# Performance work log

Hardware: AMD Instinct MI355X
Metric: run time of the kernel (lower is better)

The kernel has to match this reference:

```python
import jax, jax.numpy as jnp
import numpy as np

ACT_DIM = 768
DICT_SIZE = 32768
S0 = 4096          # top-level latent size (dict_size // prod(lower sizes))
S1 = 8             # lower_level_latent_sizes[0]
K = 64             # per-token top-k (applied globally as k * batch)


def setup_inputs() -> dict:
    key = jax.random.key(0)
    ks = jax.random.split(key, 7)
    scale_e = 1.0 / np.sqrt(ACT_DIM)
    scale_d = 1.0 / np.sqrt(DICT_SIZE)
    return {
        "x": jax.random.normal(ks[0], (4096, ACT_DIM), dtype=jnp.float32),
        "W0": jax.random.normal(ks[1], (S0, ACT_DIM), dtype=jnp.float32) * scale_e,
        "b0": jnp.zeros((S0,), dtype=jnp.float32),
        "W1": jax.random.normal(ks[2], (DICT_SIZE, ACT_DIM), dtype=jnp.float32) * scale_e,
        "b1": jnp.zeros((DICT_SIZE,), dtype=jnp.float32),
        "Wd": jax.random.normal(ks[3], (ACT_DIM, DICT_SIZE), dtype=jnp.float32) * scale_d,
        "b_dec": jnp.zeros((ACT_DIM,), dtype=jnp.float32),
    }


def reference(x, W0, b0, W1, b1, Wd, b_dec):
    B = x.shape[0]
    x_centered = x - b_dec                                   # [B, D]
    # hierarchical relu encoders
    l0 = jax.nn.relu(x_centered @ W0.T + b0)                 # [B, S0]
    l1 = jax.nn.relu(x_centered @ W1.T + b1)                 # [B, S0*S1]
    # multiplicative gating: lower-level gate broadcast over finest level
    final_dense = (l1.reshape(B, S0, S1) * l0[:, :, None]).reshape(B, S0 * S1)
    # global batch top-k over flattened [B * dict_size]
    flat = final_dense.reshape(-1)
    k_for_batch = min(K * B, flat.shape[0])
    vals, idx = jax.lax.top_k(flat, k_for_batch)
    sparse_flat = jnp.zeros_like(flat).at[idx].set(vals)
    encoded = sparse_flat.reshape(B, S0 * S1)
    # decode
    x_hat = encoded @ Wd.T + b_dec                           # [B, D]
    return x_hat
```

## Files before the change

kernel.cpp:

```cpp
#include <hip/hip_runtime.h>
#include <stdint.h>

#define DDIM 768
#define BROWS 4096
#define S0N 4096
#define DICT 32768
#define KTOT 262144u
#define PREF 2.0f
#define DELTA 4e-3f
#define CAND_CAP 8388608u
#define BAND_CAP 4096

static constexpr size_t OFF_XH   = 0;
static constexpr size_t OFF_XL   = 6291456;
static constexpr size_t OFF_W0H  = 12582912;
static constexpr size_t OFF_W0L  = 18874368;
static constexpr size_t OFF_W1H  = 25165824;
static constexpr size_t OFF_W1L  = 75497472;
static constexpr size_t OFF_WDT  = 0;
static constexpr size_t OFF_L0   = 125829120;
static constexpr size_t OFF_CTRL = 192937984;
static constexpr size_t OFF_ROWC = 193069056;
static constexpr size_t OFF_ROWD = 193085440;
static constexpr size_t OFF_CAND = 201474048;
static constexpr size_t WS_NEED  = 268582912;


typedef __attribute__((ext_vector_type(8))) short bf16x8;
typedef __attribute__((ext_vector_type(4))) float f32x4;

__device__ __forceinline__ unsigned umin_(unsigned a, unsigned b) { return a < b ? a : b; }
__device__ __forceinline__ float relu_(float v) { return v > 0.f ? v : 0.f; }

__device__ __forceinline__ unsigned short f2bf(float f) {
    union { float f; unsigned u; } v; v.f = f;
    unsigned r = v.u + 0x7FFFu + ((v.u >> 16) & 1u);
    return (unsigned short)(r >> 16);
}
__device__ __forceinline__ float bf2f(unsigned short h) {
    union { float f; unsigned u; } v; v.u = ((unsigned)h) << 16;
    return v.f;
}
__device__ __forceinline__ void split1(float a, short& h, short& l) {
    unsigned short hb = f2bf(a);
    float rem = a - bf2f(hb);
    h = (short)hb;
    l = (short)f2bf(rem);
}

__device__ __forceinline__ void gl16(const void* g, void* l) {
    __builtin_amdgcn_global_load_lds(
        (const __attribute__((address_space(1))) void*)g,
        (__attribute__((address_space(3))) void*)l,
        16, 0, 0);
}

__global__ void k_split_x(const float* __restrict__ x, const float* __restrict__ b_dec,
                          short* __restrict__ XH, short* __restrict__ XL) {
    int i = blockIdx.x * 256 + threadIdx.x;
    float4 xv = ((const float4*)x)[i];
    int d = (i % (DDIM / 4)) * 4;
    float4 bv = *(const float4*)(b_dec + d);
    float a[4] = {xv.x - bv.x, xv.y - bv.y, xv.z - bv.z, xv.w - bv.w};
    short4 h, lo;
    split1(a[0], h.x, lo.x); split1(a[1], h.y, lo.y);
    split1(a[2], h.z, lo.z); split1(a[3], h.w, lo.w);
    ((short4*)XH)[i] = h;
    ((short4*)XL)[i] = lo;
}

__global__ void k_split_w(const float* __restrict__ W, short* __restrict__ H,
                          short* __restrict__ L) {
    int i = blockIdx.x * 256 + threadIdx.x;
    float4 wv = ((const float4*)W)[i];
    short4 h, lo;
    split1(wv.x, h.x, lo.x); split1(wv.y, h.y, lo.y);
    split1(wv.z, h.z, lo.z); split1(wv.w, h.w, lo.w);
    ((short4*)H)[i] = h;
    ((short4*)L)[i] = lo;
}

__global__ void k_transpose(const float* __restrict__ Wd, float* __restrict__ WdT) {
    __shared__ float tile[32][33];
    int j0 = blockIdx.x * 32, d0 = blockIdx.y * 32;
    int tx = threadIdx.x & 31, ty = threadIdx.x >> 5;
#pragma unroll
    for (int i = 0; i < 4; ++i)
        tile[ty + i * 8][tx] = Wd[(size_t)(d0 + ty + i * 8) * DICT + j0 + tx];
    __syncthreads();
#pragma unroll
    for (int i = 0; i < 4; ++i)
        WdT[(size_t)(j0 + ty + i * 8) * DDIM + d0 + tx] = tile[tx][ty + i * 8];
}

template<int EPI>
__launch_bounds__(256, 2) __global__
void k_mm(const short* __restrict__ XH, const short* __restrict__ XL,
          const short* __restrict__ WH, const short* __restrict__ WL,
          const float* __restrict__ bias, float* __restrict__ l0buf,
          uint2* __restrict__ cand, unsigned* __restrict__ ctrl) {
    __shared__ short sAH[4096], sAL[4096], sBH[4096], sBL[4096];
    __shared__ unsigned pscan[256];
    __shared__ unsigned basev;

    const int t = threadIdx.x;
    const int w = t >> 6, l = t & 63;
    const int wm = w >> 1, wn = w & 1;
    const int bm = blockIdx.y << 7, bn = blockIdx.x << 7;

    const size_t aoff = (size_t)(bm + (t >> 2)) * DDIM + ((t & 3) << 3);
    const size_t boff = (size_t)(bn + (t >> 2)) * DDIM + ((t & 3) << 3);
    const size_t rstep = (size_t)64 * DDIM;
    short* dA0h = &sAH[t * 8]; short* dA1h = &sAH[t * 8 + 2048];
    short* dA0l = &sAL[t * 8]; short* dA1l = &sAL[t * 8 + 2048];
    short* dB0h = &sBH[t * 8]; short* dB1h = &sBH[t * 8 + 2048];
    short* dB0l = &sBL[t * 8]; short* dB1l = &sBL[t * 8 + 2048];

    f32x4 acc[4][4];
#pragma unroll
    for (int i = 0; i < 4; ++i)
#pragma unroll
        for (int j = 0; j < 4; ++j) acc[i][j] = (f32x4){0.f, 0.f, 0.f, 0.f};

    const int frow = l & 15, fkg = l >> 4;
    const int abase = (wm * 64 + frow) * 32 + fkg * 8;
    const int bbase = (wn * 64 + frow) * 32 + fkg * 8;

    for (int kt = 0; kt < DDIM / 32; ++kt) {
        __syncthreads();
        const size_t ks = (size_t)kt * 32;
        gl16(XH + aoff + ks, dA0h); gl16(XH + aoff + rstep + ks, dA1h);
        gl16(XL + aoff + ks, dA0l); gl16(XL + aoff + rstep + ks, dA1l);
        gl16(WH + boff + ks, dB0h); gl16(WH + boff + rstep + ks, dB1h);
        gl16(WL + boff + ks, dB0l); gl16(WL + boff + rstep + ks, dB1l);
        __syncthreads();

        bf16x8 ah[4], al[4], bh[4], bl[4];
#pragma unroll
        for (int i = 0; i < 4; ++i) {
            ah[i] = *(const bf16x8*)&sAH[abase + i * 512];
            al[i] = *(const bf16x8*)&sAL[abase + i * 512];
            bh[i] = *(const bf16x8*)&sBH[bbase + i * 512];
            bl[i] = *(const bf16x8*)&sBL[bbase + i * 512];
        }
#pragma unroll
        for (int i = 0; i < 4; ++i)
#pragma unroll
            for (int j = 0; j < 4; ++j)
                acc[i][j] = __builtin_amdgcn_mfma_f32_16x16x32_bf16(ah[i], bh[j], acc[i][j], 0, 0, 0);
#pragma unroll
        for (int i = 0; i < 4; ++i)
#pragma unroll
            for (int j = 0; j < 4; ++j)
                acc[i][j] = __builtin_amdgcn_mfma_f32_16x16x32_bf16(ah[i], bl[j], acc[i][j], 0, 0, 0);
#pragma unroll
        for (int i = 0; i < 4; ++i)
#pragma unroll
            for (int j = 0; j < 4; ++j)
                acc[i][j] = __builtin_amdgcn_mfma_f32_16x16x32_bf16(al[i], bh[j], acc[i][j], 0, 0, 0);
    }

    if constexpr (EPI == 0) {
#pragma unroll
        for (int i = 0; i < 4; ++i) {
#pragma unroll
            for (int r = 0; r < 4; ++r) {
                int row = bm + wm * 64 + i * 16 + fkg * 4 + r;
                float* orow = l0buf + (size_t)row * S0N;
#pragma unroll
                for (int j = 0; j < 4; ++j) {
                    int col = bn + wn * 64 + j * 16 + frow;
                    orow[col] = relu_(acc[i][j][r] + bias[col]);
                }
            }
        }
    } else {
        unsigned cnt = 0;
#pragma unroll
        for (int i = 0; i < 4; ++i)
#pragma unroll
            for (int j = 0; j < 4; ++j)
#pragma unroll
                for (int r = 0; r < 4; ++r) {
                    int row = bm + wm * 64 + i * 16 + fkg * 4 + r;
                    int col = bn + wn * 64 + j * 16 + frow;
                    float v = relu_(acc[i][j][r] + bias[col]);
                    v *= l0buf[(size_t)row * S0N + (col >> 3)];
                    acc[i][j][r] = v;
                    cnt += (v >= PREF) ? 1u : 0u;
                }
        pscan[t] = cnt;
        __syncthreads();
        for (int s = 1; s < 256; s <<= 1) {
            unsigned v2 = (t >= s) ? pscan[t - s] : 0u;
            __syncthreads();
            pscan[t] += v2;
            __syncthreads();
        }
        if (t == 255) basev = atomicAdd(&ctrl[0], pscan[255]);
        __syncthreads();
        unsigned off = basev + pscan[t] - cnt;
#pragma unroll
        for (int i = 0; i < 4; ++i)
#pragma unroll
            for (int j = 0; j < 4; ++j)
#pragma unroll
                for (int r = 0; r < 4; ++r) {
                    float v = acc[i][j][r];
                    if (v >= PREF) {
                        int row = bm + wm * 64 + i * 16 + fkg * 4 + r;
                        int col = bn + wn * 64 + j * 16 + frow;
                        if (off < CAND_CAP)
                            cand[off] = make_uint2(__float_as_uint(v),
                                                   ((unsigned)row << 15) | (unsigned)col);
                        ++off;
                    }
                }
    }
}

__global__ void k_hist1(const uint2* __restrict__ cand, unsigned* __restrict__ ctrl) {
    __shared__ unsigned h[2048];
    for (int i = threadIdx.x; i < 2048; i += 256) h[i] = 0;
    __syncthreads();
    unsigned n = umin_(ctrl[0], CAND_CAP);
    for (unsigned i = blockIdx.x * 256 + threadIdx.x; i < n; i += gridDim.x * 256)
        atomicAdd(&h[cand[i].x >> 20], 1u);
    __syncthreads();
    unsigned* hist = ctrl + 256;
    for (int i = threadIdx.x; i < 2048; i += 256)
        if (h[i]) atomicAdd(&hist[i], h[i]);
}

__global__ void k_scan1(unsigned* __restrict__ ctrl) {
    __shared__ unsigned hs[2048];
    __shared__ unsigned cs[256];
    const unsigned* h = ctrl + 256;
    int t = threadIdx.x;
    for (int i = t; i < 2048; i += 256) hs[i] = h[i];
    __syncthreads();
    unsigned s = 0;
    for (int b = 0; b < 8; ++b) s += hs[t * 8 + b];
    cs[t] = s;
    __syncthreads();
    if (t == 0) {
        unsigned cum = 0, T = 0, cb = 0;
        for (int c = 255; c >= 0; --c) {
            if (cum + cs[c] >= KTOT) {
                for (int b = c * 8 + 7; b >= c * 8; --b) {
                    cum += hs[b];
                    if (cum >= KTOT) { T = (unsigned)b; cb = cum - hs[b]; break; }
                }
                break;
            }
            cum += cs[c];
        }
        ctrl[1] = T; ctrl[2] = cb;
    }
}

__global__ void k_hist2(const uint2* __restrict__ cand, unsigned* __restrict__ ctrl) {
    unsigned n = umin_(ctrl[0], CAND_CAP);
    unsigned T = ctrl[1];
    unsigned* hist2 = ctrl + 2304;
    for (unsigned i = blockIdx.x * 256 + threadIdx.x; i < n; i += gridDim.x * 256) {
        unsigned u = cand[i].x;
        if ((u >> 20) == T) atomicAdd(&hist2[(u >> 8) & 0xFFFu], 1u);
    }
}

__global__ void k_scan2(unsigned* __restrict__ ctrl) {
    __shared__ unsigned hs[4096];
    __shared__ unsigned cs[256];
    const unsigned* h = ctrl + 2304;
    int t = threadIdx.x;
    for (int i = t; i < 4096; i += 256) hs[i] = h[i];
    __syncthreads();
    unsigned s = 0;
    for (int b = 0; b < 16; ++b) s += hs[t * 16 + b];
    cs[t] = s;
    __syncthreads();
    if (t == 0) {
        unsigned cum = ctrl[2], T2 = 0;
        for (int c = 255; c >= 0; --c) {
            if (cum + cs[c] >= KTOT) {
                for (int b = c * 16 + 15; b >= c * 16; --b) {
                    cum += hs[b];
                    if (cum >= KTOT) { T2 = (unsigned)b; break; }
                }
                break;
            }
            cum += cs[c];
        }
        ctrl[3] = (ctrl[1] << 12) | T2;
    }
}

__global__ void k_band(const uint2* __restrict__ cand, unsigned* __restrict__ ctrl) {
    __shared__ unsigned lhi;
    if (threadIdx.x == 0) lhi = 0;
    __syncthreads();
    unsigned n = umin_(ctrl[0], CAND_CAP);
    unsigned H = ctrl[3];
    float lo = __uint_as_float(H << 8) - DELTA;
    float hi = __uint_as_float((H + 1u) << 8) + DELTA;
    unsigned* band_idx = ctrl + 6400;
    unsigned my = 0;
    for (unsigned i = blockIdx.x * 256 + threadIdx.x; i < n; i += gridDim.x * 256) {
        float v = __uint_as_float(cand[i].x);
        if (v > hi) ++my;
        else if (v >= lo) {
            unsigned p = atomicAdd(&ctrl[5], 1u);
            if (p < BAND_CAP) band_idx[p] = cand[i].y;
        }
    }
    atomicAdd(&lhi, my);
    __syncthreads();
    if (threadIdx.x == 0 && lhi) atomicAdd(&ctrl[4], lhi);
}

__global__ void k_f64(const float* __restrict__ x, const float* __restrict__ b_dec,
                      const float* __restrict__ W0, const float* __restrict__ b0,
                      const float* __restrict__ W1, const float* __restrict__ b1,
                      const unsigned* __restrict__ ctrl, double* __restrict__ band_v) {
    unsigned n = umin_(ctrl[5], BAND_CAP);
    unsigned bi = blockIdx.x;
    if (bi >= n) return;
    const unsigned* band_idx = ctrl + 6400;
    unsigned idx = band_idx[bi];
    int b = idx >> 15, j = idx & 32767, s0 = j >> 3;
    int lane = threadIdx.x;
    const float* xr = x + (size_t)b * DDIM;
    const float* w1 = W1 + (size_t)j * DDIM;
    const float* w0 = W0 + (size_t)s0 * DDIM;
    double d1 = 0.0, d0 = 0.0;
    for (int k = lane; k < DDIM; k += 64) {
        double xv = (double)xr[k] - (double)b_dec[k];
        d1 += xv * (double)w1[k];
        d0 += xv * (double)w0[k];
    }
    for (int off = 32; off; off >>= 1) {
        d1 += __shfl_down(d1, off);
        d0 += __shfl_down(d0, off);
    }
    if (lane == 0) {
        double l1v = d1 + (double)b1[j];  l1v = l1v > 0.0 ? l1v : 0.0;
        double l0v = d0 + (double)b0[s0]; l0v = l0v > 0.0 ? l0v : 0.0;
        band_v[bi] = l1v * l0v;
    }
}

__global__ void k_final(unsigned* __restrict__ ctrl, const double* __restrict__ band_v,
                        uint2* __restrict__ extra) {
    __shared__ unsigned long long skey[BAND_CAP];
    __shared__ unsigned sidx[BAND_CAP];
    int t = threadIdx.x;
    unsigned n = umin_(ctrl[5], BAND_CAP);
    const unsigned* band_idx = ctrl + 6400;
    for (int i = t; i < BAND_CAP; i += 256) {
        if ((unsigned)i < n) {
            skey[i] = (unsigned long long)__double_as_longlong(band_v[i]);
            sidx[i] = band_idx[i];
        } else {
            skey[i] = 0ull; sidx[i] = 0xFFFFFFFFu;
        }
    }
    __syncthreads();
    for (int kk = 2; kk <= BAND_CAP; kk <<= 1) {
        for (int jj = kk >> 1; jj > 0; jj >>= 1) {
            for (int i = t; i < BAND_CAP; i += 256) {
                int ixj = i ^ jj;
                if (ixj > i) {
                    unsigned long long ka = skey[i], kb = skey[ixj];
                    unsigned ia = sidx[i], ib = sidx[ixj];
                    bool ab = (ka > kb) || (ka == kb && ia < ib);
                    bool asc = ((i & kk) == 0);
                    if (asc ? !ab : ab) {
                        skey[i] = kb; skey[ixj] = ka;
                        sidx[i] = ib; sidx[ixj] = ia;
                    }
                }
            }
            __syncthreads();
        }
    }
    unsigned c_hi = ctrl[4];
    unsigned k_rem = (c_hi < KTOT) ? (KTOT - c_hi) : 0u;
    if (k_rem > n) k_rem = n;
    if (t == 0) ctrl[6] = k_rem;
    for (unsigned i = t; i < k_rem; i += 256)
        extra[i] = make_uint2(sidx[i],
                              __float_as_uint((float)__longlong_as_double((long long)skey[i])));
}

__global__ void k_rows_a(const uint2* __restrict__ cand, const unsigned* __restrict__ ctrl,
                         unsigned* __restrict__ rowc, uint2* __restrict__ rowd) {
    unsigned n = umin_(ctrl[0], CAND_CAP);
    unsigned H = ctrl[3];
    float hi = __uint_as_float((H + 1u) << 8) + DELTA;
    for (unsigned i = blockIdx.x * 256 + threadIdx.x; i < n; i += gridDim.x * 256) {
        unsigned u = cand[i].x;
        if (__uint_as_float(u) > hi) {
            unsigned idx = cand[i].y;
            unsigned b = idx >> 15;
            unsigned p = atomicAdd(&rowc[b], 1u);
            if (p < 256u) rowd[(b << 8) + p] = make_uint2(idx & 32767u, u);
        }
    }
}

__global__ void k_rows_b(const unsigned* __restrict__ ctrl, const uint2* __restrict__ extra,
                         unsigned* __restrict__ rowc, uint2* __restrict__ rowd) {
    unsigned k_rem = ctrl[6];
    for (unsigned i = blockIdx.x * 256 + threadIdx.x; i < k_rem; i += gridDim.x * 256) {
        unsigned idx = extra[i].x;
        unsigned b = idx >> 15;
        unsigned p = atomicAdd(&rowc[b], 1u);
        if (p < 256u) rowd[(b << 8) + p] = make_uint2(idx & 32767u, extra[i].y);
    }
}

__launch_bounds__(256) __global__
void k_decode(const uint2* __restrict__ rowd, const unsigned* __restrict__ rowc,
              const float* __restrict__ WdT, const float* __restrict__ b_dec,
              float* __restrict__ out) {
    __shared__ uint2 e[256];
    int b = blockIdx.x, t = threadIdx.x;
    unsigned c = rowc[b]; if (c > 256u) c = 256u;
    if ((unsigned)t < c) e[t] = rowd[(b << 8) + t];
    __syncthreads();
    float a0 = b_dec[t], a1 = b_dec[t + 256], a2 = b_dec[t + 512];
#pragma unroll 4
    for (unsigned i = 0; i < c; ++i) {
        float v = __uint_as_float(e[i].y);
        const float* w = WdT + (size_t)e[i].x * DDIM;
        a0 = fmaf(v, w[t], a0);
        a1 = fmaf(v, w[t + 256], a1);
        a2 = fmaf(v, w[t + 512], a2);
    }
    float* o = out + (size_t)b * DDIM;
    o[t] = a0; o[t + 256] = a1; o[t + 512] = a2;
}

extern "C" void kernel_launch(void* const* d_in, const int* in_sizes, int n_in,
                              void* d_out, int out_size, void* d_ws, size_t ws_size,
                              hipStream_t stream) {
    const float* x     = (const float*)d_in[0];
    const float* W0    = (const float*)d_in[1];
    const float* b0    = (const float*)d_in[2];
    const float* W1    = (const float*)d_in[3];
    const float* b1    = (const float*)d_in[4];
    const float* Wd    = (const float*)d_in[5];
    const float* b_dec = (const float*)d_in[6];
    float* out = (float*)d_out;

    if (ws_size < WS_NEED) {
        hipMemsetAsync(d_out, 0, (size_t)out_size * sizeof(float), stream);
        return;
    }

    char* ws = (char*)d_ws;
    short*    XH     = (short*)(ws + OFF_XH);
    short*    XL     = (short*)(ws + OFF_XL);
    short*    W0H    = (short*)(ws + OFF_W0H);
    short*    W0L    = (short*)(ws + OFF_W0L);
    short*    W1H    = (short*)(ws + OFF_W1H);
    short*    W1L    = (short*)(ws + OFF_W1L);
    float*    WdT    = (float*)(ws + OFF_WDT);
    float*    l0     = (float*)(ws + OFF_L0);
    unsigned* ctrl   = (unsigned*)(ws + OFF_CTRL);
    double*   band_v = (double*)(ws + OFF_CTRL + 65536);
    uint2*    extra  = (uint2*)(ws + OFF_CTRL + 98304);
    unsigned* rowc   = (unsigned*)(ws + OFF_ROWC);
    uint2*    rowd   = (uint2*)(ws + OFF_ROWD);
    uint2*    cand   = (uint2*)(ws + OFF_CAND);

    hipMemsetAsync(ctrl, 0, 6400 * sizeof(unsigned), stream);
    hipMemsetAsync(rowc, 0, BROWS * sizeof(unsigned), stream);

    k_split_x<<<(BROWS * DDIM / 4) / 256, 256, 0, stream>>>(x, b_dec, XH, XL);
    k_split_w<<<(S0N * DDIM / 4) / 256, 256, 0, stream>>>(W0, W0H, W0L);
    k_split_w<<<(DICT * DDIM / 4) / 256, 256, 0, stream>>>(W1, W1H, W1L);

    k_mm<0><<<dim3(S0N / 128, BROWS / 128), 256, 0, stream>>>(XH, XL, W0H, W0L, b0, l0, nullptr, nullptr);
    k_mm<1><<<dim3(DICT / 128, BROWS / 128), 256, 0, stream>>>(XH, XL, W1H, W1L, b1, l0, cand, ctrl);

    k_transpose<<<dim3(DICT / 32, DDIM / 32), 256, 0, stream>>>(Wd, WdT);

    k_hist1<<<1024, 256, 0, stream>>>(cand, ctrl);
    k_scan1<<<1, 256, 0, stream>>>(ctrl);
    k_hist2<<<1024, 256, 0, stream>>>(cand, ctrl);
    k_scan2<<<1, 256, 0, stream>>>(ctrl);
    k_band<<<1024, 256, 0, stream>>>(cand, ctrl);
    k_f64<<<BAND_CAP, 64, 0, stream>>>(x, b_dec, W0, b0, W1, b1, ctrl, band_v);
    k_final<<<1, 256, 0, stream>>>(ctrl, band_v, extra);

    k_rows_a<<<1024, 256, 0, stream>>>(cand, ctrl, rowc, rowd);
    k_rows_b<<<32, 256, 0, stream>>>(ctrl, extra, rowc, rowd);
    k_decode<<<BROWS, 256, 0, stream>>>(rowd, rowc, WdT, b_dec, out);
}
```

Before: 1.352 ms.

## Rewrite split-bf16 GEMM with 256x256 tiles, double-buffered LDS and swizzled grid

The encoder GEMM kernel moves from 128x128 tiles with 256 threads to 256x256 tiles with 512 threads and 8x4 MFMA accumulators per wave. Global-to-LDS loads are double-buffered with K=64 stages, so the next stage is fetched while the current one computes. The three split-precision products (hi*hi, hi*lo, lo*hi) are now run as 36 sequential K-phases instead of being interleaved per step. Blocks are remapped with an XCD-style swizzle to improve L2 locality. The cost is 128KB of LDS per block and lower occupancy, and the epilogue scan now spans 512 threads.

```diff
diff --git a/kernel.cpp b/kernel.cpp
--- a/kernel.cpp
+++ b/kernel.cpp
@@ -94,122 +94,150 @@
 }
 
 template<int EPI>
-__launch_bounds__(256, 2) __global__
+__launch_bounds__(512, 2) __global__
 void k_mm(const short* __restrict__ XH, const short* __restrict__ XL,
           const short* __restrict__ WH, const short* __restrict__ WL,
           const float* __restrict__ bias, float* __restrict__ l0buf,
           uint2* __restrict__ cand, unsigned* __restrict__ ctrl) {
-    __shared__ short sAH[4096], sAL[4096], sBH[4096], sBL[4096];
-    __shared__ unsigned pscan[256];
-    __shared__ unsigned basev;
+    __shared__ __align__(16) char smem[131072];
 
     const int t = threadIdx.x;
     const int w = t >> 6, l = t & 63;
-    const int wm = w >> 1, wn = w & 1;
-    const int bm = blockIdx.y << 7, bn = blockIdx.x << 7;
-
-    const size_t aoff = (size_t)(bm + (t >> 2)) * DDIM + ((t & 3) << 3);
-    const size_t boff = (size_t)(bn + (t >> 2)) * DDIM + ((t & 3) << 3);
-    const size_t rstep = (size_t)64 * DDIM;
-    short* dA0h = &sAH[t * 8]; short* dA1h = &sAH[t * 8 + 2048];
-    short* dA0l = &sAL[t * 8]; short* dA1l = &sAL[t * 8 + 2048];
-    short* dB0h = &sBH[t * 8]; short* dB1h = &sBH[t * 8 + 2048];
-    short* dB0l = &sBL[t * 8]; short* dB1l = &sBL[t * 8 + 2048];
-
-    f32x4 acc[4][4];
-#pragma unroll
-    for (int i = 0; i < 4; ++i)
+    const int wm = w >> 2, wn = w & 3;
+    const int lr = l & 15, lk = l >> 4;
+
+    const int nwg = gridDim.x;
+    const int bid = blockIdx.x;
+    const int swz = (bid & 7) * (nwg >> 3) + (bid >> 3);
+    const int bm = (swz & 15) << 8;
+    const int bn = (swz >> 4) << 8;
+
+    unsigned idxA[4], idxB[4];
+#pragma unroll
+    for (int q = 0; q < 4; ++q) {
+        const int ab = w * 4 + q;
+        idxA[q] = (unsigned)(bm + (ab >> 4) * 128 + ((ab >> 1) & 7) * 16 + lr) * 768u
+                + (unsigned)((ab & 1) * 32 + lk * 8);
+        idxB[q] = (unsigned)(bn + (ab >> 3) * 64 + ((ab >> 1) & 3) * 16 + lr) * 768u
+                + (unsigned)((ab & 1) * 32 + lk * 8);
+    }
+
+    f32x4 acc[8][4];
+#pragma unroll
+    for (int i = 0; i < 8; ++i)
 #pragma unroll
         for (int j = 0; j < 4; ++j) acc[i][j] = (f32x4){0.f, 0.f, 0.f, 0.f};
 
-    const int frow = l & 15, fkg = l >> 4;
-    const int abase = (wm * 64 + frow) * 32 + fkg * 8;
-    const int bbase = (wn * 64 + frow) * 32 + fkg * 8;
-
-    for (int kt = 0; kt < DDIM / 32; ++kt) {
-        __syncthreads();
-        const size_t ks = (size_t)kt * 32;
-        gl16(XH + aoff + ks, dA0h); gl16(XH + aoff + rstep + ks, dA1h);
-        gl16(XL + aoff + ks, dA0l); gl16(XL + aoff + rstep + ks, dA1l);
-        gl16(WH + boff + ks, dB0h); gl16(WH + boff + rstep + ks, dB1h);
-        gl16(WL + boff + ks, dB0l); gl16(WL + boff + rstep + ks, dB1l);
-        __syncthreads();
-
-        bf16x8 ah[4], al[4], bh[4], bl[4];
-#pragma unroll
-        for (int i = 0; i < 4; ++i) {
-            ah[i] = *(const bf16x8*)&sAH[abase + i * 512];
-            al[i] = *(const bf16x8*)&sAL[abase + i * 512];
-            bh[i] = *(const bf16x8*)&sBH[bbase + i * 512];
-            bl[i] = *(const bf16x8*)&sBL[bbase + i * 512];
-        }
-#pragma unroll
-        for (int i = 0; i < 4; ++i)
-#pragma unroll
-            for (int j = 0; j < 4; ++j)
-                acc[i][j] = __builtin_amdgcn_mfma_f32_16x16x32_bf16(ah[i], bh[j], acc[i][j], 0, 0, 0);
-#pragma unroll
-        for (int i = 0; i < 4; ++i)
-#pragma unroll
-            for (int j = 0; j < 4; ++j)
-                acc[i][j] = __builtin_amdgcn_mfma_f32_16x16x32_bf16(ah[i], bl[j], acc[i][j], 0, 0, 0);
-#pragma unroll
-        for (int i = 0; i < 4; ++i)
-#pragma unroll
-            for (int j = 0; j < 4; ++j)
-                acc[i][j] = __builtin_amdgcn_mfma_f32_16x16x32_bf16(al[i], bh[j], acc[i][j], 0, 0, 0);
-    }
+#pragma unroll
+    for (int q = 0; q < 4; ++q) {
+        gl16(XH + idxA[q], smem + (w * 4 + q) * 1024);
+        gl16(WH + idxB[q], smem + 65536 + (w * 4 + q) * 1024);
+    }
+    asm volatile("s_waitcnt vmcnt(0)" ::: "memory");
+    __syncthreads();
+
+    int cur = 0;
+    for (int kt = 0; kt < 36; ++kt) {
+        const int ktn = kt + 1;
+        const bool hn = ktn < 36;
+        const short* An; const short* Bn; unsigned kbn;
+        if (ktn < 12)      { An = XH; Bn = WH; kbn = (unsigned)ktn * 64u; }
+        else if (ktn < 24) { An = XH; Bn = WL; kbn = (unsigned)(ktn - 12) * 64u; }
+        else               { An = XL; Bn = WH; kbn = (unsigned)(ktn - 24) * 64u; }
+        char* stA = smem + (cur ^ 1) * 32768;
+        char* stB = smem + 65536 + (cur ^ 1) * 32768;
+        const short* rA = (const short*)(smem + cur * 32768);
+        const short* rB = (const short*)(smem + 65536 + cur * 32768);
+
+        bf16x8 bf[4];
+#pragma unroll
+        for (int p = 0; p < 4; ++p) {
+            const int ks = p >> 1, mh = p & 1;
+            bf16x8 af[4];
+#pragma unroll
+            for (int m2 = 0; m2 < 4; ++m2) {
+                const int mi = mh * 4 + m2;
+                af[m2] = *(const bf16x8*)(rA + ((wm * 16 + mi * 2 + ks) * 1024 + l * 16) / 2);
+            }
+            if (mh == 0) {
+#pragma unroll
+                for (int nj = 0; nj < 4; ++nj)
+                    bf[nj] = *(const bf16x8*)(rB + ((wn * 8 + nj * 2 + ks) * 1024 + l * 16) / 2);
+            }
+            if (hn) {
+                gl16(An + idxA[p] + kbn, stA + (w * 4 + p) * 1024);
+                gl16(Bn + idxB[p] + kbn, stB + (w * 4 + p) * 1024);
+            }
+            __builtin_amdgcn_s_barrier();
+            asm volatile("s_waitcnt lgkmcnt(0)" ::: "memory");
+            __builtin_amdgcn_sched_barrier(0);
+            __builtin_amdgcn_s_setprio(1);
+#pragma unroll
+            for (int m2 = 0; m2 < 4; ++m2)
+#pragma unroll
+                for (int nj = 0; nj < 4; ++nj)
+                    acc[mh * 4 + m2][nj] = __builtin_amdgcn_mfma_f32_16x16x32_bf16(
+                        af[m2], bf[nj], acc[mh * 4 + m2][nj], 0, 0, 0);
+            __builtin_amdgcn_s_setprio(0);
+            __builtin_amdgcn_s_barrier();
+        }
+        asm volatile("s_waitcnt vmcnt(0)" ::: "memory");
+        __builtin_amdgcn_s_barrier();
+        cur ^= 1;
+    }
+    __syncthreads();
 
     if constexpr (EPI == 0) {
 #pragma unroll
-        for (int i = 0; i < 4; ++i) {
+        for (int mi = 0; mi < 8; ++mi) {
 #pragma unroll
             for (int r = 0; r < 4; ++r) {
-                int row = bm + wm * 64 + i * 16 + fkg * 4 + r;
+                const int row = bm + wm * 128 + mi * 16 + lk * 4 + r;
                 float* orow = l0buf + (size_t)row * S0N;
 #pragma unroll
-                for (int j = 0; j < 4; ++j) {
-                    int col = bn + wn * 64 + j * 16 + frow;
-                    orow[col] = relu_(acc[i][j][r] + bias[col]);
+                for (int nj = 0; nj < 4; ++nj) {
+                    const int col = bn + wn * 64 + nj * 16 + lr;
+                    orow[col] = relu_(acc[mi][nj][r] + bias[col]);
                 }
             }
         }
     } else {
+        unsigned* pscan = (unsigned*)smem;
         unsigned cnt = 0;
 #pragma unroll
-        for (int i = 0; i < 4; ++i)
-#pragma unroll
-            for (int j = 0; j < 4; ++j)
+        for (int mi = 0; mi < 8; ++mi)
+#pragma unroll
+            for (int nj = 0; nj < 4; ++nj)
 #pragma unroll
                 for (int r = 0; r < 4; ++r) {
-                    int row = bm + wm * 64 + i * 16 + fkg * 4 + r;
-                    int col = bn + wn * 64 + j * 16 + frow;
-                    float v = relu_(acc[i][j][r] + bias[col]);
+                    const int row = bm + wm * 128 + mi * 16 + lk * 4 + r;
+                    const int col = bn + wn * 64 + nj * 16 + lr;
+                    float v = relu_(acc[mi][nj][r] + bias[col]);
                     v *= l0buf[(size_t)row * S0N + (col >> 3)];
-                    acc[i][j][r] = v;
+                    acc[mi][nj][r] = v;
                     cnt += (v >= PREF) ? 1u : 0u;
                 }
         pscan[t] = cnt;
         __syncthreads();
-        for (int s = 1; s < 256; s <<= 1) {
+        for (int s = 1; s < 512; s <<= 1) {
             unsigned v2 = (t >= s) ? pscan[t - s] : 0u;
             __syncthreads();
             pscan[t] += v2;
             __syncthreads();
         }
-        if (t == 255) basev = atomicAdd(&ctrl[0], pscan[255]);
+        if (t == 511) pscan[512] = atomicAdd(&ctrl[0], pscan[511]);
         __syncthreads();
-        unsigned off = basev + pscan[t] - cnt;
-#pragma unroll
-        for (int i = 0; i < 4; ++i)
-#pragma unroll
-            for (int j = 0; j < 4; ++j)
+        unsigned off = pscan[512] + pscan[t] - cnt;
+#pragma unroll
+        for (int mi = 0; mi < 8; ++mi)
+#pragma unroll
+            for (int nj = 0; nj < 4; ++nj)
 #pragma unroll
                 for (int r = 0; r < 4; ++r) {
-                    float v = acc[i][j][r];
+                    const float v = acc[mi][nj][r];
                     if (v >= PREF) {
-                        int row = bm + wm * 64 + i * 16 + fkg * 4 + r;
-                        int col = bn + wn * 64 + j * 16 + frow;
+                        const int row = bm + wm * 128 + mi * 16 + lk * 4 + r;
+                        const int col = bn + wn * 64 + nj * 16 + lr;
                         if (off < CAND_CAP)
                             cand[off] = make_uint2(__float_as_uint(v),
                                                    ((unsigned)row << 15) | (unsigned)col);
@@ -482,8 +510,8 @@
     k_split_w<<<(S0N * DDIM / 4) / 256, 256, 0, stream>>>(W0, W0H, W0L);
     k_split_w<<<(DICT * DDIM / 4) / 256, 256, 0, stream>>>(W1, W1H, W1L);
 
-    k_mm<0><<<dim3(S0N / 128, BROWS / 128), 256, 0, stream>>>(XH, XL, W0H, W0L, b0, l0, nullptr, nullptr);
-    k_mm<1><<<dim3(DICT / 128, BROWS / 128), 256, 0, stream>>>(XH, XL, W1H, W1L, b1, l0, cand, ctrl);
+    k_mm<0><<<(S0N / 256) * 16, 512, 0, stream>>>(XH, XL, W0H, W0L, b0, l0, nullptr, nullptr);
+    k_mm<1><<<(DICT / 256) * 16, 512, 0, stream>>>(XH, XL, W1H, W1L, b1, l0, cand, ctrl);
 
     k_transpose<<<dim3(DICT / 32, DDIM / 32), 256, 0, stream>>>(Wd, WdT);
 
```

After: 1.310 ms. 1.03x faster.
